# Optimization experiments

Measured on AMD Instinct MI355X. Metric: run time of the kernel, lower is better.

## Reference

```python
import jax, jax.numpy as jnp
import numpy as np

N_A = 50000
N_B = 50000
E = 800000
C_IN = 128
C_OUT = 128


def _lstm_cell_seq1(x, W_ih, b):
    # PyTorch LSTM with seq_len=1 and zero initial state: h = o*tanh(i*g)
    # gate order in weight_ih: [i, f, g, o]; f-gate is unused since c0 = 0.
    gates = x @ W_ih.T + b  # [N, 4H]
    i, f, g, o = jnp.split(gates, 4, axis=-1)
    c = jax.nn.sigmoid(i) * jnp.tanh(g)
    return jax.nn.sigmoid(o) * jnp.tanh(c)


def _conv(x_src, x_dst, edge_index, W_ih, b_lstm, W_lin, b_lin):
    # LSTM message depends only on src features -> compute per node, gather per edge.
    msg = _lstm_cell_seq1(x_src, W_ih, b_lstm)          # [N_src, C_OUT]
    src, dst = edge_index[0], edge_index[1]
    aggr = jax.ops.segment_sum(msg[src], dst, num_segments=x_dst.shape[0])  # [N_dst, C_OUT]
    h = jnp.concatenate([x_dst, aggr], axis=-1)          # [N_dst, C_IN + C_OUT]
    return jax.nn.relu(h @ W_lin.T + b_lin)              # dropout = identity (eval mode)


def setup_inputs() -> dict:
    key = jax.random.key(0)
    ks = jax.random.split(key, 12)
    s = 0.05
    return {
        "x_a": jax.random.normal(ks[0], (N_A, C_IN), jnp.float32),
        "x_b": jax.random.normal(ks[1], (N_B, C_IN), jnp.float32),
        "edge_ab": jax.random.randint(ks[2], (2, E), 0, 50000, jnp.int64 if jax.config.jax_enable_x64 else jnp.int32),
        "edge_ba": jax.random.randint(ks[3], (2, E), 0, 50000, jnp.int64 if jax.config.jax_enable_x64 else jnp.int32),
        "W_ih_ab": jax.random.normal(ks[4], (4 * C_OUT, C_IN), jnp.float32) * s,
        "b_ab": jax.random.normal(ks[5], (4 * C_OUT,), jnp.float32) * s,
        "W_lin_ab": jax.random.normal(ks[6], (C_OUT, C_IN + C_OUT), jnp.float32) * s,
        "b_lin_ab": jax.random.normal(ks[7], (C_OUT,), jnp.float32) * s,
        "W_ih_ba": jax.random.normal(ks[8], (4 * C_OUT, C_IN), jnp.float32) * s,
        "b_ba": jax.random.normal(ks[9], (4 * C_OUT,), jnp.float32) * s,
        "W_lin_ba": jax.random.normal(ks[10], (C_OUT, C_IN + C_OUT), jnp.float32) * s,
        "b_lin_ba": jax.random.normal(ks[11], (C_OUT,), jnp.float32) * s,
    }


def reference(x_a, x_b, edge_ab, edge_ba,
              W_ih_ab, b_ab, W_lin_ab, b_lin_ab,
              W_ih_ba, b_ba, W_lin_ba, b_lin_ba):
    # a_to_b relation updates type_b nodes; b_to_a updates type_a nodes.
    out_b = _conv(x_a, x_b, edge_ab, W_ih_ab, b_ab, W_lin_ab, b_lin_ab)
    out_a = _conv(x_b, x_a, edge_ba, W_ih_ba, b_ba, W_lin_ba, b_lin_ba)
    # stack (same shapes) => [2, N, C_OUT]: index 0 = new x_a, index 1 = new x_b
    return jnp.stack([out_a, out_b], axis=0)
```

## Files before the change

kernel.cpp:

```cpp
#include <hip/hip_runtime.h>
#include <cstdint>
#include <cstddef>

#define CCH 128
#define TK 4096
#define FCAP 5120
#define SLOT 5120
#define MAXBKT 512
#define XPAD 136
#define APAD 264

typedef __attribute__((ext_vector_type(8))) short short8;
typedef __attribute__((ext_vector_type(4))) float floatx4;

__device__ __forceinline__ unsigned short f2bf(float f) {
    unsigned u = __builtin_bit_cast(unsigned, f);
    u += 0x7fffu + ((u >> 16) & 1u);
    return (unsigned short)(u >> 16);
}
__device__ __forceinline__ float bf2f(unsigned short h) {
    unsigned u = ((unsigned)h) << 16;
    return __builtin_bit_cast(float, u);
}
__device__ __forceinline__ float sigmoidf_(float x) { return 1.0f / (1.0f + __expf(-x)); }
__device__ __forceinline__ float tanh_fast(float x) {
    x = fminf(fmaxf(x, -10.0f), 10.0f);
    float e = __expf(2.0f * x);
    return (e - 1.0f) / (e + 1.0f);
}

__global__ __launch_bounds__(256) void prep_weights_kernel(
    const float* __restrict__ Wih0, const float* __restrict__ Wih1,
    const float* __restrict__ Wlin0, const float* __restrict__ Wlin1,
    unsigned short* __restrict__ frag_ih, unsigned short* __restrict__ frag_lin,
    int* __restrict__ btot, int NBKT)
{
    int t = blockIdx.x * 256 + threadIdx.x;
    if (t < 12288) {
        int l  = t & 63;
        int kc = (t >> 6) & 3;
        int ct = (t >> 8) & 7;
        int g  = (t >> 11) % 3;
        int rel = t / 6144;
        int gb = (g == 0) ? 0 : (g == 1 ? 256 : 384);
        const float* W = rel ? Wih1 : Wih0;
        int n  = gb + ct * 16 + (l & 15);
        int kb = kc * 32 + (l >> 4) * 8;
        unsigned short* o = frag_ih + (size_t)t * 8;
#pragma unroll
        for (int j = 0; j < 8; j++) o[j] = f2bf(W[(size_t)n * CCH + kb + j]);
    } else if (t < 20480) {
        int t2 = t - 12288;
        int l  = t2 & 63;
        int kc = (t2 >> 6) & 7;
        int ct = (t2 >> 9) & 7;
        int rel = t2 >> 12;
        const float* W = rel ? Wlin1 : Wlin0;
        int n  = ct * 16 + (l & 15);
        int kb = kc * 32 + (l >> 4) * 8;
        unsigned short* o = frag_lin + (size_t)t2 * 8;
#pragma unroll
        for (int j = 0; j < 8; j++) o[j] = f2bf(W[(size_t)n * 256 + kb + j]);
    } else {
        int z = t - 20480;
        if (z < NBKT) btot[z] = 0;
    }
}

__global__ __launch_bounds__(256) void lstm_scatter_kernel(
    const float* __restrict__ x0, const float* __restrict__ x1,
    const unsigned short* __restrict__ wfrag,
    const float* __restrict__ b0, const float* __restrict__ b1,
    unsigned short* __restrict__ msg0, unsigned short* __restrict__ msg1,
    int N0, int N1, int nblk0,
    const int* __restrict__ src0, const int* __restrict__ dst0,
    const int* __restrict__ src1, const int* __restrict__ dst1,
    int* __restrict__ btot, unsigned* __restrict__ packed,
    int E0, int E1, int nbkt0, int NBKT, int nT)
{
    __shared__ unsigned short xs[32 * XPAD];
    __shared__ int h[MAXBKT];
    __shared__ int cur[MAXBKT];
    const int tid = threadIdx.x;

    if (blockIdx.x < nT) {
        for (int i = tid; i < NBKT; i += 256) h[i] = 0;
        __syncthreads();
        const long long Etot = (long long)E0 + E1;
        const long long base = (long long)blockIdx.x * TK;
        int gg[16];
        unsigned pk[16];
#pragma unroll
        for (int j = 0; j < 16; j++) {
            long long e = base + j * 256 + tid;
            gg[j] = -1;
            if (e < Etot) {
                int s, d, g;
                if (e < E0) { d = dst0[e]; s = src0[e]; g = d >> 8; }
                else { long long ee = e - E0; d = dst1[ee]; s = src1[ee]; g = nbkt0 + (d >> 8); }
                gg[j] = g;
                pk[j] = ((unsigned)(d & 255) << 24) | (unsigned)s;
                atomicAdd(&h[g], 1);
            }
        }
        __syncthreads();
        for (int i = tid; i < NBKT; i += 256) {
            int c = h[i];
            cur[i] = i * SLOT + (c ? atomicAdd(&btot[i], c) : 0);
        }
        __syncthreads();
#pragma unroll
        for (int j = 0; j < 16; j++) {
            if (gg[j] >= 0) {
                int pos = atomicAdd(&cur[gg[j]], 1);
                packed[pos] = pk[j];
            }
        }
        return;
    }

    const int lb = blockIdx.x - nT;
    const int rel = (lb >= nblk0);
    const int nb = (rel ? (lb - nblk0) : lb) * 32;
    const float* x = rel ? x1 : x0;
    const float* bias = rel ? b1 : b0;
    unsigned short* msg = rel ? msg1 : msg0;
    const int N = rel ? N1 : N0;
    const unsigned short* wf = wfrag + (size_t)rel * 6144 * 8;

    {
        int r = tid >> 3;
        int c0 = (tid & 7) * 16;
        int n = nb + r;
        unsigned short* dstp = xs + r * XPAD + c0;
        if (n < N) {
            const float4* srcp = (const float4*)(x + (size_t)n * CCH + c0);
#pragma unroll
            for (int qq = 0; qq < 4; qq++) {
                float4 v = srcp[qq];
                unsigned u0 = (unsigned)f2bf(v.x) | ((unsigned)f2bf(v.y) << 16);
                unsigned u1 = (unsigned)f2bf(v.z) | ((unsigned)f2bf(v.w) << 16);
                *(uint2*)(dstp + qq * 4) = make_uint2(u0, u1);
            }
        } else {
#pragma unroll
            for (int qq = 0; qq < 4; qq++) *(uint2*)(dstp + qq * 4) = make_uint2(0u, 0u);
        }
    }
    __syncthreads();

    const int w = tid >> 6;
    const int l = tid & 63;
    const int ctb2 = w * 2;
    const int q = l >> 4;
    const int m16 = l & 15;

    floatx4 acc[3][2][2];
#pragma unroll
    for (int g = 0; g < 3; g++)
#pragma unroll
        for (int c = 0; c < 2; c++)
#pragma unroll
            for (int mt = 0; mt < 2; mt++) acc[g][c][mt] = (floatx4){0.f, 0.f, 0.f, 0.f};

    const unsigned short* arow0 = xs + m16 * XPAD + q * 8;
    const unsigned short* arow1 = xs + (16 + m16) * XPAD + q * 8;
#pragma unroll
    for (int kc = 0; kc < 4; kc++) {
        short8 af0 = *(const short8*)(arow0 + kc * 32);
        short8 af1 = *(const short8*)(arow1 + kc * 32);
#pragma unroll
        for (int g = 0; g < 3; g++)
#pragma unroll
            for (int c = 0; c < 2; c++) {
                const unsigned short* bp = wf + ((((size_t)g * 8 + (ctb2 + c)) * 4 + kc) * 64 + l) * 8;
                short8 bv = *(const short8*)bp;
                acc[g][c][0] = __builtin_amdgcn_mfma_f32_16x16x32_bf16(af0, bv, acc[g][c][0], 0, 0, 0);
                acc[g][c][1] = __builtin_amdgcn_mfma_f32_16x16x32_bf16(af1, bv, acc[g][c][1], 0, 0, 0);
            }
    }

    __syncthreads();
#pragma unroll
    for (int c = 0; c < 2; c++) {
        const int col = (ctb2 + c) * 16 + m16;
        const float bi = bias[col], bg = bias[256 + col], bo = bias[384 + col];
#pragma unroll
        for (int mt = 0; mt < 2; mt++)
#pragma unroll
            for (int r = 0; r < 4; r++) {
                const int nl = mt * 16 + q * 4 + r;
                float iv = sigmoidf_(acc[0][c][mt][r] + bi);
                float gv = tanh_fast(acc[1][c][mt][r] + bg);
                float ov = sigmoidf_(acc[2][c][mt][r] + bo);
                xs[nl * XPAD + col] = f2bf(ov * tanh_fast(iv * gv));
            }
    }
    __syncthreads();
    {
        int r = tid >> 3;
        int c0 = (tid & 7) * 16;
        int n = nb + r;
        if (n < N) {
            const unsigned short* srow = xs + r * XPAD + c0;
            uint4 v0 = *(const uint4*)(srow);
            uint4 v1 = *(const uint4*)(srow + 8);
            unsigned short* drow = msg + (size_t)n * CCH + c0;
            *(uint4*)(drow) = v0;
            *(uint4*)(drow + 8) = v1;
        }
    }
}

__global__ __launch_bounds__(512) void fine_sort_kernel(
    unsigned* __restrict__ packed, const int* __restrict__ btot,
    int* __restrict__ offs0, int* __restrict__ deg0,
    int* __restrict__ offs1, int* __restrict__ deg1,
    int N0, int N1, int nbkt0)
{
    __shared__ unsigned pin[FCAP];
    __shared__ int hist[256], scn[256], cur[256];
    const int g = blockIdx.x;
    const int tid = threadIdx.x;
    const int base = g * SLOT;
    const int cnt = min(btot[g], FCAP);

    for (int i = tid; i < cnt; i += 512) pin[i] = packed[base + i];
    if (tid < 256) hist[tid] = 0;
    __syncthreads();
    for (int i = tid; i < cnt; i += 512) atomicAdd(&hist[pin[i] >> 24], 1);
    __syncthreads();
    int v = (tid < 256) ? hist[tid] : 0;
    if (tid < 256) scn[tid] = v;
    __syncthreads();
    for (int off = 1; off < 256; off <<= 1) {
        int t = (tid >= off && tid < 256) ? scn[tid - off] : 0;
        __syncthreads();
        if (tid < 256) scn[tid] += t;
        __syncthreads();
    }
    if (tid < 256) {
        int excl = scn[tid] - v;
        cur[tid] = excl;
        const int rel = (g >= nbkt0);
        const int lb = rel ? g - nbkt0 : g;
        const int n = lb * 256 + tid;
        const int N = rel ? N1 : N0;
        if (n < N) {
            if (rel) { offs1[n] = base + excl; deg1[n] = v; }
            else     { offs0[n] = base + excl; deg0[n] = v; }
        }
    }
    __syncthreads();
    int* op = (int*)packed;
    for (int i = tid; i < cnt; i += 512) {
        unsigned p = pin[i];
        int pos = atomicAdd(&cur[p >> 24], 1);
        op[base + pos] = (int)(p & 0x00FFFFFFu);
    }
}

__global__ __launch_bounds__(512) void gather_linear_kernel(
    const float* __restrict__ xd0, const float* __restrict__ xd1,
    const unsigned short* __restrict__ msg0, const unsigned short* __restrict__ msg1,
    const int* __restrict__ csr,
    const int* __restrict__ offs0, const int* __restrict__ offs1,
    const int* __restrict__ deg0, const int* __restrict__ deg1,
    const unsigned short* __restrict__ wfrag,
    const float* __restrict__ bl0, const float* __restrict__ bl1,
    float* __restrict__ out0, float* __restrict__ out1,
    int P0, int P1, int N0, int N1)
{
    __shared__ unsigned short s[32 * APAD];
    const int tid = threadIdx.x;
    const int grp = blockIdx.x >> 3;
    const int sub = blockIdx.x & 7;
    const int rel = (sub >> 2) & 1;
    const int lb = grp * 4 + (sub & 3);
    const int P = rel ? P1 : P0;
    if (lb >= P) return;
    const int nb = lb * 32;
    const float* xd = rel ? xd1 : xd0;
    const unsigned short* msg = rel ? msg1 : msg0;
    const int* offs = rel ? offs1 : offs0;
    const int* deg = rel ? deg1 : deg0;
    const float* bl = rel ? bl1 : bl0;
    float* outp = rel ? out1 : out0;
    const int N = rel ? N1 : N0;
    const unsigned short* wf = wfrag + (size_t)rel * 4096 * 8;

    {
        int r = tid >> 4;
        int c0 = (tid & 15) * 8;
        int n = nb + r;
        unsigned short* drow = s + r * APAD + c0;
        if (n < N) {
            const floatx4* srcp = (const floatx4*)(xd + (size_t)n * CCH + c0);
            floatx4 v0 = __builtin_nontemporal_load(srcp);
            floatx4 v1 = __builtin_nontemporal_load(srcp + 1);
            uint4 u;
            u.x = (unsigned)f2bf(v0[0]) | ((unsigned)f2bf(v0[1]) << 16);
            u.y = (unsigned)f2bf(v0[2]) | ((unsigned)f2bf(v0[3]) << 16);
            u.z = (unsigned)f2bf(v1[0]) | ((unsigned)f2bf(v1[1]) << 16);
            u.w = (unsigned)f2bf(v1[2]) | ((unsigned)f2bf(v1[3]) << 16);
            *(uint4*)drow = u;
        } else {
            *(uint4*)drow = make_uint4(0u, 0u, 0u, 0u);
        }
    }
    {
        const int w = tid >> 6;
        const int l = tid & 63;
        const int g = l >> 4;
        const int c = l & 15;
        const int nloc = w * 4 + g;
        const int n = nb + nloc;
        float a0 = 0.f, a1 = 0.f, a2 = 0.f, a3 = 0.f;
        float a4 = 0.f, a5 = 0.f, a6 = 0.f, a7 = 0.f;
        if (n < N) {
            const int start = offs[n];
            const int cnt = deg[n];
            const int* ce = csr + start;
            const unsigned short* mb = msg + c * 8;
#define ACC8(U) { \
            a0 += bf2f((unsigned short)(U.x)); a1 += bf2f((unsigned short)((U.x) >> 16)); \
            a2 += bf2f((unsigned short)(U.y)); a3 += bf2f((unsigned short)((U.y) >> 16)); \
            a4 += bf2f((unsigned short)(U.z)); a5 += bf2f((unsigned short)((U.z) >> 16)); \
            a6 += bf2f((unsigned short)(U.w)); a7 += bf2f((unsigned short)((U.w) >> 16)); }
            int j = 0;
            if (cnt >= 4) {
                int s0 = ce[0], s1 = ce[1], s2 = ce[2], s3 = ce[3];
                for (; j + 8 <= cnt; j += 4) {
                    uint4 u0 = *(const uint4*)(mb + (size_t)s0 * CCH);
                    uint4 u1 = *(const uint4*)(mb + (size_t)s1 * CCH);
                    uint4 u2 = *(const uint4*)(mb + (size_t)s2 * CCH);
                    uint4 u3 = *(const uint4*)(mb + (size_t)s3 * CCH);
                    s0 = ce[j + 4]; s1 = ce[j + 5]; s2 = ce[j + 6]; s3 = ce[j + 7];
                    ACC8(u0); ACC8(u1); ACC8(u2); ACC8(u3);
                }
                uint4 u0 = *(const uint4*)(mb + (size_t)s0 * CCH);
                uint4 u1 = *(const uint4*)(mb + (size_t)s1 * CCH);
                uint4 u2 = *(const uint4*)(mb + (size_t)s2 * CCH);
                uint4 u3 = *(const uint4*)(mb + (size_t)s3 * CCH);
                ACC8(u0); ACC8(u1); ACC8(u2); ACC8(u3);
                j += 4;
            }
            for (; j < cnt; j++) {
                uint4 u0 = *(const uint4*)(mb + (size_t)ce[j] * CCH);
                ACC8(u0);
            }
#undef ACC8
        }
        uint4 o;
        o.x = (unsigned)f2bf(a0) | ((unsigned)f2bf(a1) << 16);
        o.y = (unsigned)f2bf(a2) | ((unsigned)f2bf(a3) << 16);
        o.z = (unsigned)f2bf(a4) | ((unsigned)f2bf(a5) << 16);
        o.w = (unsigned)f2bf(a6) | ((unsigned)f2bf(a7) << 16);
        *(uint4*)(s + nloc * APAD + CCH + c * 8) = o;
    }
    __syncthreads();

    const int w = tid >> 6;
    const int l = tid & 63;
    const int q = l >> 4;
    const int m16 = l & 15;

    floatx4 acc[2];
    acc[0] = (floatx4){0.f, 0.f, 0.f, 0.f};
    acc[1] = (floatx4){0.f, 0.f, 0.f, 0.f};

    const unsigned short* arow0 = s + m16 * APAD + q * 8;
    const unsigned short* arow1 = s + (16 + m16) * APAD + q * 8;
#pragma unroll
    for (int kc = 0; kc < 8; kc++) {
        short8 af0 = *(const short8*)(arow0 + kc * 32);
        short8 af1 = *(const short8*)(arow1 + kc * 32);
        const unsigned short* bp = wf + ((((size_t)w) * 8 + kc) * 64 + l) * 8;
        short8 bv = *(const short8*)bp;
        acc[0] = __builtin_amdgcn_mfma_f32_16x16x32_bf16(af0, bv, acc[0], 0, 0, 0);
        acc[1] = __builtin_amdgcn_mfma_f32_16x16x32_bf16(af1, bv, acc[1], 0, 0, 0);
    }

    const int col = w * 16 + m16;
    const float bv = bl[col];
#pragma unroll
    for (int mt = 0; mt < 2; mt++)
#pragma unroll
        for (int r = 0; r < 4; r++) {
            const int node = nb + mt * 16 + q * 4 + r;
            if (node < N) {
                float v = fmaxf(acc[mt][r] + bv, 0.0f);
                __builtin_nontemporal_store(v, &outp[(size_t)node * CCH + col]);
            }
        }
}

extern "C" void kernel_launch(void* const* d_in, const int* in_sizes, int n_in,
                              void* d_out, int out_size, void* d_ws, size_t ws_size,
                              hipStream_t stream) {
    const float* x_a      = (const float*)d_in[0];
    const float* x_b      = (const float*)d_in[1];
    const int*   e_ab     = (const int*)d_in[2];
    const int*   e_ba     = (const int*)d_in[3];
    const float* W_ih_ab  = (const float*)d_in[4];
    const float* b_ab     = (const float*)d_in[5];
    const float* W_lin_ab = (const float*)d_in[6];
    const float* b_lin_ab = (const float*)d_in[7];
    const float* W_ih_ba  = (const float*)d_in[8];
    const float* b_ba     = (const float*)d_in[9];
    const float* W_lin_ba = (const float*)d_in[10];
    const float* b_lin_ba = (const float*)d_in[11];

    const int NA = in_sizes[0] / CCH;
    const int NB = in_sizes[1] / CCH;
    const int E0 = in_sizes[2] / 2;
    const int E1 = in_sizes[3] / 2;

    float* out = (float*)d_out;
    char* ws = (char*)d_ws;
    size_t off = 0;
    auto alloc = [&](size_t bytes) { char* p = ws + off; off += (bytes + 255) & ~(size_t)255; return p; };

    unsigned short* wfrag_ih  = (unsigned short*)alloc(12288 * 8 * 2);
    unsigned short* wfrag_lin = (unsigned short*)alloc(8192 * 8 * 2);
    unsigned short* msg_a     = (unsigned short*)alloc((size_t)NA * CCH * 2);
    unsigned short* msg_b     = (unsigned short*)alloc((size_t)NB * CCH * 2);

    const int nbkt0 = (NB + 255) / 256;
    const int nbkt1 = (NA + 255) / 256;
    const int NBKT = nbkt0 + nbkt1;
    const long long Etot = (long long)E0 + E1;
    const int nT = (int)((Etot + TK - 1) / TK);

    int* btot   = (int*)alloc((size_t)NBKT * 4);
    int* offs_b = (int*)alloc((size_t)NB * 4);
    int* offs_a = (int*)alloc((size_t)NA * 4);
    int* deg_b  = (int*)alloc((size_t)NB * 4);
    int* deg_a  = (int*)alloc((size_t)NA * 4);
    unsigned* packed = (unsigned*)alloc((size_t)NBKT * SLOT * 4);

    const int nblkA = (NA + 31) / 32;
    const int nblkB = (NB + 31) / 32;

    prep_weights_kernel<<<82, 256, 0, stream>>>(
        W_ih_ab, W_ih_ba, W_lin_ab, W_lin_ba, wfrag_ih, wfrag_lin, btot, NBKT);

    lstm_scatter_kernel<<<nT + nblkA + nblkB, 256, 0, stream>>>(
        x_a, x_b, wfrag_ih, b_ab, b_ba, msg_a, msg_b, NA, NB, nblkA,
        e_ab, e_ab + E0, e_ba, e_ba + E1, btot, packed, E0, E1, nbkt0, NBKT, nT);

    fine_sort_kernel<<<NBKT, 512, 0, stream>>>(
        packed, btot, offs_b, deg_b, offs_a, deg_a, NB, NA, nbkt0);

    const int Pmax = (nblkB > nblkA) ? nblkB : nblkA;
    const int G = ((Pmax + 3) / 4) * 8;
    gather_linear_kernel<<<G, 512, 0, stream>>>(
        x_b, x_a, msg_a, msg_b, (const int*)packed,
        offs_b, offs_a, deg_b, deg_a, wfrag_lin, b_lin_ab, b_lin_ba,
        out + (size_t)NA * CCH, out, nblkB, nblkA, NB, NA);
}
```

Measured before the change: 235.8 us.

## Split each node's edge gather across two thread groups with LDS reduction

The gather+linear kernel now handles 16 destination nodes per block instead of 32. Two 16-lane groups split each node's neighbor list in half and combine their partial sums through a shared-memory buffer before the bf16 MFMA linear layer. The aim is to shorten the per-thread serial gather chain and to launch twice as many blocks for better latency hiding. In exchange it adds an extra barrier and LDS traffic, and each block now does only a single MFMA tile per wave with the weight fragments reloaded twice as often overall.

```diff
diff --git a/kernel.cpp b/kernel.cpp
--- a/kernel.cpp
+++ b/kernel.cpp
@@ -271,7 +271,8 @@
     float* __restrict__ out0, float* __restrict__ out1,
     int P0, int P1, int N0, int N1)
 {
-    __shared__ unsigned short s[32 * APAD];
+    __shared__ unsigned short s[16 * APAD];
+    __shared__ float part[16 * 128];
     const int tid = threadIdx.x;
     const int grp = blockIdx.x >> 3;
     const int sub = blockIdx.x & 7;
@@ -279,7 +280,7 @@
     const int lb = grp * 4 + (sub & 3);
     const int P = rel ? P1 : P0;
     if (lb >= P) return;
-    const int nb = lb * 32;
+    const int nb = lb * 16;
     const float* xd = rel ? xd1 : xd0;
     const unsigned short* msg = rel ? msg1 : msg0;
     const int* offs = rel ? offs1 : offs0;
@@ -290,37 +291,37 @@
     const unsigned short* wf = wfrag + (size_t)rel * 4096 * 8;
 
     {
-        int r = tid >> 4;
-        int c0 = (tid & 15) * 8;
+        int r = tid >> 5;
+        int c0 = (tid & 31) * 4;
         int n = nb + r;
         unsigned short* drow = s + r * APAD + c0;
         if (n < N) {
             const floatx4* srcp = (const floatx4*)(xd + (size_t)n * CCH + c0);
             floatx4 v0 = __builtin_nontemporal_load(srcp);
-            floatx4 v1 = __builtin_nontemporal_load(srcp + 1);
-            uint4 u;
+            uint2 u;
             u.x = (unsigned)f2bf(v0[0]) | ((unsigned)f2bf(v0[1]) << 16);
             u.y = (unsigned)f2bf(v0[2]) | ((unsigned)f2bf(v0[3]) << 16);
-            u.z = (unsigned)f2bf(v1[0]) | ((unsigned)f2bf(v1[1]) << 16);
-            u.w = (unsigned)f2bf(v1[2]) | ((unsigned)f2bf(v1[3]) << 16);
-            *(uint4*)drow = u;
+            *(uint2*)drow = u;
         } else {
-            *(uint4*)drow = make_uint4(0u, 0u, 0u, 0u);
+            *(uint2*)drow = make_uint2(0u, 0u);
         }
     }
     {
         const int w = tid >> 6;
         const int l = tid & 63;
-        const int g = l >> 4;
+        const int gidx = w * 4 + (l >> 4);
+        const int nloc = gidx >> 1;
+        const int half = gidx & 1;
         const int c = l & 15;
-        const int nloc = w * 4 + g;
         const int n = nb + nloc;
         float a0 = 0.f, a1 = 0.f, a2 = 0.f, a3 = 0.f;
         float a4 = 0.f, a5 = 0.f, a6 = 0.f, a7 = 0.f;
         if (n < N) {
             const int start = offs[n];
             const int cnt = deg[n];
-            const int* ce = csr + start;
+            const int hh = cnt >> 1;
+            const int* ce = csr + start + (half ? hh : 0);
+            const int myCnt = half ? (cnt - hh) : hh;
             const unsigned short* mb = msg + c * 8;
 #define ACC8(U) { \
             a0 += bf2f((unsigned short)(U.x)); a1 += bf2f((unsigned short)((U.x) >> 16)); \
@@ -328,9 +329,9 @@
             a4 += bf2f((unsigned short)(U.z)); a5 += bf2f((unsigned short)((U.z) >> 16)); \
             a6 += bf2f((unsigned short)(U.w)); a7 += bf2f((unsigned short)((U.w) >> 16)); }
             int j = 0;
-            if (cnt >= 4) {
+            if (myCnt >= 4) {
                 int s0 = ce[0], s1 = ce[1], s2 = ce[2], s3 = ce[3];
-                for (; j + 8 <= cnt; j += 4) {
+                for (; j + 8 <= myCnt; j += 4) {
                     uint4 u0 = *(const uint4*)(mb + (size_t)s0 * CCH);
                     uint4 u1 = *(const uint4*)(mb + (size_t)s1 * CCH);
                     uint4 u2 = *(const uint4*)(mb + (size_t)s2 * CCH);
@@ -345,18 +346,31 @@
                 ACC8(u0); ACC8(u1); ACC8(u2); ACC8(u3);
                 j += 4;
             }
-            for (; j < cnt; j++) {
+            for (; j < myCnt; j++) {
                 uint4 u0 = *(const uint4*)(mb + (size_t)ce[j] * CCH);
                 ACC8(u0);
             }
 #undef ACC8
         }
-        uint4 o;
-        o.x = (unsigned)f2bf(a0) | ((unsigned)f2bf(a1) << 16);
-        o.y = (unsigned)f2bf(a2) | ((unsigned)f2bf(a3) << 16);
-        o.z = (unsigned)f2bf(a4) | ((unsigned)f2bf(a5) << 16);
-        o.w = (unsigned)f2bf(a6) | ((unsigned)f2bf(a7) << 16);
-        *(uint4*)(s + nloc * APAD + CCH + c * 8) = o;
+        if (half) {
+            float* pp = part + nloc * 128 + c * 8;
+            *(floatx4*)pp = (floatx4){a0, a1, a2, a3};
+            *(floatx4*)(pp + 4) = (floatx4){a4, a5, a6, a7};
+        }
+        __syncthreads();
+        if (!half) {
+            const float* pp = part + nloc * 128 + c * 8;
+            floatx4 p0 = *(const floatx4*)pp;
+            floatx4 p1 = *(const floatx4*)(pp + 4);
+            a0 += p0[0]; a1 += p0[1]; a2 += p0[2]; a3 += p0[3];
+            a4 += p1[0]; a5 += p1[1]; a6 += p1[2]; a7 += p1[3];
+            uint4 o;
+            o.x = (unsigned)f2bf(a0) | ((unsigned)f2bf(a1) << 16);
+            o.y = (unsigned)f2bf(a2) | ((unsigned)f2bf(a3) << 16);
+            o.z = (unsigned)f2bf(a4) | ((unsigned)f2bf(a5) << 16);
+            o.w = (unsigned)f2bf(a6) | ((unsigned)f2bf(a7) << 16);
+            *(uint4*)(s + nloc * APAD + CCH + c * 8) = o;
+        }
     }
     __syncthreads();
 
@@ -365,34 +379,26 @@
     const int q = l >> 4;
     const int m16 = l & 15;
 
-    floatx4 acc[2];
-    acc[0] = (floatx4){0.f, 0.f, 0.f, 0.f};
-    acc[1] = (floatx4){0.f, 0.f, 0.f, 0.f};
-
+    floatx4 acc = (floatx4){0.f, 0.f, 0.f, 0.f};
     const unsigned short* arow0 = s + m16 * APAD + q * 8;
-    const unsigned short* arow1 = s + (16 + m16) * APAD + q * 8;
 #pragma unroll
     for (int kc = 0; kc < 8; kc++) {
         short8 af0 = *(const short8*)(arow0 + kc * 32);
-        short8 af1 = *(const short8*)(arow1 + kc * 32);
         const unsigned short* bp = wf + ((((size_t)w) * 8 + kc) * 64 + l) * 8;
         short8 bv = *(const short8*)bp;
-        acc[0] = __builtin_amdgcn_mfma_f32_16x16x32_bf16(af0, bv, acc[0], 0, 0, 0);
-        acc[1] = __builtin_amdgcn_mfma_f32_16x16x32_bf16(af1, bv, acc[1], 0, 0, 0);
+        acc = __builtin_amdgcn_mfma_f32_16x16x32_bf16(af0, bv, acc, 0, 0, 0);
     }
 
     const int col = w * 16 + m16;
     const float bv = bl[col];
 #pragma unroll
-    for (int mt = 0; mt < 2; mt++)
-#pragma unroll
-        for (int r = 0; r < 4; r++) {
-            const int node = nb + mt * 16 + q * 4 + r;
-            if (node < N) {
-                float v = fmaxf(acc[mt][r] + bv, 0.0f);
-                __builtin_nontemporal_store(v, &outp[(size_t)node * CCH + col]);
-            }
-        }
+    for (int r = 0; r < 4; r++) {
+        const int node = nb + q * 4 + r;
+        if (node < N) {
+            float v = fmaxf(acc[r] + bv, 0.0f);
+            __builtin_nontemporal_store(v, &outp[(size_t)node * CCH + col]);
+        }
+    }
 }
 
 extern "C" void kernel_launch(void* const* d_in, const int* in_sizes, int n_in,
@@ -441,6 +447,8 @@
 
     const int nblkA = (NA + 31) / 32;
     const int nblkB = (NB + 31) / 32;
+    const int nblkA16 = (NA + 15) / 16;
+    const int nblkB16 = (NB + 15) / 16;
 
     prep_weights_kernel<<<82, 256, 0, stream>>>(
         W_ih_ab, W_ih_ba, W_lin_ab, W_lin_ba, wfrag_ih, wfrag_lin, btot, NBKT);
@@ -452,10 +460,10 @@
     fine_sort_kernel<<<NBKT, 512, 0, stream>>>(
         packed, btot, offs_b, deg_b, offs_a, deg_a, NB, NA, nbkt0);
 
-    const int Pmax = (nblkB > nblkA) ? nblkB : nblkA;
+    const int Pmax = (nblkB16 > nblkA16) ? nblkB16 : nblkA16;
     const int G = ((Pmax + 3) / 4) * 8;
     gather_linear_kernel<<<G, 512, 0, stream>>>(
         x_b, x_a, msg_a, msg_b, (const int*)packed,
         offs_b, offs_a, deg_b, deg_a, wfrag_lin, b_lin_ab, b_lin_ba,
-        out + (size_t)NA * CCH, out, nblkB, nblkA, NB, NA);
-}
+        out + (size_t)NA * CCH, out, nblkB16, nblkA16, NB, NA);
+}
```

Result: slower. 245.8 us (+4.2%).

## Sort destination nodes by degree within buckets to balance gather waves

Applied to the files above, without the earlier changes.

The fine sort kernel now builds a per-256-node-bucket permutation that orders destination nodes by in-degree, using a counting sort over degrees clamped to 63. The gather-linear kernel processes nodes in permuted order, so the 16-lane groups in each wavefront handle nodes of similar degree and less time is lost to divergence in the edge loop. In exchange there is an extra indirection for loads and stores, the output rows of a block are scattered across a 256-node range rather than contiguous, and the sort kernel gains more shared-memory scans and barriers.

```diff
diff --git a/kernel.cpp b/kernel.cpp
--- a/kernel.cpp
+++ b/kernel.cpp
@@ -216,10 +216,12 @@
     unsigned* __restrict__ packed, const int* __restrict__ btot,
     int* __restrict__ offs0, int* __restrict__ deg0,
     int* __restrict__ offs1, int* __restrict__ deg1,
+    int* __restrict__ perm0, int* __restrict__ perm1,
     int N0, int N1, int nbkt0)
 {
     __shared__ unsigned pin[FCAP];
     __shared__ int hist[256], scn[256], cur[256];
+    __shared__ int dhist[64], dscan[64], dcur[64];
     const int g = blockIdx.x;
     const int tid = threadIdx.x;
     const int base = g * SLOT;
@@ -227,6 +229,7 @@
 
     for (int i = tid; i < cnt; i += 512) pin[i] = packed[base + i];
     if (tid < 256) hist[tid] = 0;
+    if (tid < 64) dhist[tid] = 0;
     __syncthreads();
     for (int i = tid; i < cnt; i += 512) atomicAdd(&hist[pin[i] >> 24], 1);
     __syncthreads();
@@ -239,17 +242,35 @@
         if (tid < 256) scn[tid] += t;
         __syncthreads();
     }
+    const int rel = (g >= nbkt0);
+    const int lb = rel ? g - nbkt0 : g;
+    const int n = lb * 256 + tid;
+    const int N = rel ? N1 : N0;
+    const bool valid = (tid < 256) && (n < N);
     if (tid < 256) {
         int excl = scn[tid] - v;
         cur[tid] = excl;
-        const int rel = (g >= nbkt0);
-        const int lb = rel ? g - nbkt0 : g;
-        const int n = lb * 256 + tid;
-        const int N = rel ? N1 : N0;
-        if (n < N) {
+        if (valid) {
             if (rel) { offs1[n] = base + excl; deg1[n] = v; }
             else     { offs0[n] = base + excl; deg0[n] = v; }
         }
+    }
+    if (valid) atomicAdd(&dhist[min(v, 63)], 1);
+    __syncthreads();
+    if (tid < 64) dscan[tid] = dhist[tid];
+    __syncthreads();
+    for (int off = 1; off < 64; off <<= 1) {
+        int t = (tid >= off && tid < 64) ? dscan[tid - off] : 0;
+        __syncthreads();
+        if (tid < 64) dscan[tid] += t;
+        __syncthreads();
+    }
+    if (tid < 64) dcur[tid] = dscan[tid] - dhist[tid];
+    __syncthreads();
+    if (valid) {
+        int rank = atomicAdd(&dcur[min(v, 63)], 1);
+        if (rel) perm1[lb * 256 + rank] = n;
+        else     perm0[lb * 256 + rank] = n;
     }
     __syncthreads();
     int* op = (int*)packed;
@@ -266,6 +287,7 @@
     const int* __restrict__ csr,
     const int* __restrict__ offs0, const int* __restrict__ offs1,
     const int* __restrict__ deg0, const int* __restrict__ deg1,
+    const int* __restrict__ perm0, const int* __restrict__ perm1,
     const unsigned short* __restrict__ wfrag,
     const float* __restrict__ bl0, const float* __restrict__ bl1,
     float* __restrict__ out0, float* __restrict__ out1,
@@ -284,6 +306,7 @@
     const unsigned short* msg = rel ? msg1 : msg0;
     const int* offs = rel ? offs1 : offs0;
     const int* deg = rel ? deg1 : deg0;
+    const int* perm = rel ? perm1 : perm0;
     const float* bl = rel ? bl1 : bl0;
     float* outp = rel ? out1 : out0;
     const int N = rel ? N1 : N0;
@@ -292,10 +315,11 @@
     {
         int r = tid >> 4;
         int c0 = (tid & 15) * 8;
-        int n = nb + r;
+        int slot = nb + r;
         unsigned short* drow = s + r * APAD + c0;
-        if (n < N) {
-            const floatx4* srcp = (const floatx4*)(xd + (size_t)n * CCH + c0);
+        if (slot < N) {
+            int node = perm[slot];
+            const floatx4* srcp = (const floatx4*)(xd + (size_t)node * CCH + c0);
             floatx4 v0 = __builtin_nontemporal_load(srcp);
             floatx4 v1 = __builtin_nontemporal_load(srcp + 1);
             uint4 u;
@@ -314,12 +338,13 @@
         const int g = l >> 4;
         const int c = l & 15;
         const int nloc = w * 4 + g;
-        const int n = nb + nloc;
+        const int slot = nb + nloc;
         float a0 = 0.f, a1 = 0.f, a2 = 0.f, a3 = 0.f;
         float a4 = 0.f, a5 = 0.f, a6 = 0.f, a7 = 0.f;
-        if (n < N) {
-            const int start = offs[n];
-            const int cnt = deg[n];
+        if (slot < N) {
+            const int node = perm[slot];
+            const int start = offs[node];
+            const int cnt = deg[node];
             const int* ce = csr + start;
             const unsigned short* mb = msg + c * 8;
 #define ACC8(U) { \
@@ -387,8 +412,9 @@
     for (int mt = 0; mt < 2; mt++)
 #pragma unroll
         for (int r = 0; r < 4; r++) {
-            const int node = nb + mt * 16 + q * 4 + r;
-            if (node < N) {
+            const int slot = nb + mt * 16 + q * 4 + r;
+            if (slot < N) {
+                int node = perm[slot];
                 float v = fmaxf(acc[mt][r] + bv, 0.0f);
                 __builtin_nontemporal_store(v, &outp[(size_t)node * CCH + col]);
             }
@@ -437,6 +463,8 @@
     int* offs_a = (int*)alloc((size_t)NA * 4);
     int* deg_b  = (int*)alloc((size_t)NB * 4);
     int* deg_a  = (int*)alloc((size_t)NA * 4);
+    int* perm_b = (int*)alloc((size_t)nbkt0 * 256 * 4);
+    int* perm_a = (int*)alloc((size_t)nbkt1 * 256 * 4);
     unsigned* packed = (unsigned*)alloc((size_t)NBKT * SLOT * 4);
 
     const int nblkA = (NA + 31) / 32;
@@ -450,12 +478,12 @@
         e_ab, e_ab + E0, e_ba, e_ba + E1, btot, packed, E0, E1, nbkt0, NBKT, nT);
 
     fine_sort_kernel<<<NBKT, 512, 0, stream>>>(
-        packed, btot, offs_b, deg_b, offs_a, deg_a, NB, NA, nbkt0);
+        packed, btot, offs_b, deg_b, offs_a, deg_a, perm_b, perm_a, NB, NA, nbkt0);
 
     const int Pmax = (nblkB > nblkA) ? nblkB : nblkA;
     const int G = ((Pmax + 3) / 4) * 8;
     gather_linear_kernel<<<G, 512, 0, stream>>>(
         x_b, x_a, msg_a, msg_b, (const int*)packed,
-        offs_b, offs_a, deg_b, deg_a, wfrag_lin, b_lin_ab, b_lin_ba,
+        offs_b, offs_a, deg_b, deg_a, perm_b, perm_a, wfrag_lin, b_lin_ab, b_lin_ba,
         out + (size_t)NA * CCH, out, nblkB, nblkA, NB, NA);
 }
```

Result: slower. 243.0 us (+3.0%).
